# Optimization experiments

Measured on AMD Instinct MI355X. Metric: run time of the kernel, lower is better.

The kernel has to match this reference:

```python
import jax, jax.numpy as jnp
import numpy as np

N_NODES = 100000
N_EDGES = 1600000
IN_CH = 128
HID = 128
OUT_CH = 64
N_GRAPHS = 256


def setup_inputs() -> dict:
    key = jax.random.key(0)
    ks = jax.random.split(key, 12)
    x = jax.random.normal(ks[0], (N_NODES, IN_CH), dtype=jnp.float32)
    edge_index = jax.random.randint(ks[1], (2, N_EDGES), 0, N_NODES, dtype=jnp.int64)
    batch = jnp.sort(jax.random.randint(ks[2], (N_NODES,), 0, N_GRAPHS, dtype=jnp.int64))
    def glorot(k, shape):
        lim = np.sqrt(6.0 / (shape[0] + shape[1]))
        return jax.random.uniform(k, shape, jnp.float32, -lim, lim)
    w1 = glorot(ks[3], (IN_CH, HID)); b1 = jnp.zeros((HID,), jnp.float32)
    w2 = glorot(ks[4], (HID, HID));   b2 = jnp.zeros((HID,), jnp.float32)
    w3 = glorot(ks[5], (HID, HID));   b3 = jnp.zeros((HID,), jnp.float32)
    w_out = glorot(ks[6], (HID, OUT_CH)); b_out = jnp.zeros((OUT_CH,), jnp.float32)
    return {"x": x, "edge_index": edge_index, "batch": batch,
            "w1": w1, "b1": b1, "w2": w2, "b2": b2, "w3": w3, "b3": b3,
            "w_out": w_out, "b_out": b_out}


def reference(x, edge_index, batch, w1, b1, w2, b2, w3, b3, w_out, b_out):
    N = x.shape[0]
    # GCN normalization with added self-loops (PyG gcn_norm, symmetric):
    loop = jnp.arange(N, dtype=edge_index.dtype)
    src = jnp.concatenate([edge_index[0], loop])  # message source
    dst = jnp.concatenate([edge_index[1], loop])  # aggregate at target
    deg = jax.ops.segment_sum(jnp.ones(src.shape, jnp.float32), dst, num_segments=N)
    dinv = jax.lax.rsqrt(jnp.maximum(deg, 1.0))  # deg >= 1 due to self-loops
    norm = dinv[src] * dinv[dst]  # [E+N]

    def gcn_conv(h, w, b):
        h = h @ w  # transform first (PyG order)
        agg = jax.ops.segment_sum(norm[:, None] * h[src], dst, num_segments=N)
        return agg + b

    # norm module is None, dropout p=0 -> act-only branch, dropout no-op
    h = jax.nn.relu(gcn_conv(x, w1, b1))
    h = jax.nn.relu(gcn_conv(h, w2, b2))
    h = jax.nn.relu(gcn_conv(h, w3, b3))

    # global mean pool over graphs
    cnt = jax.ops.segment_sum(jnp.ones((N,), jnp.float32), batch, num_segments=N_GRAPHS)
    pooled = jax.ops.segment_sum(h, batch, num_segments=N_GRAPHS) / jnp.maximum(cnt, 1.0)[:, None]
    return pooled @ w_out + b_out  # [N_GRAPHS, OUT_CH]
```

## Files before the change

### kernel.cpp

```cpp
#include <hip/hip_runtime.h>
#include <hip/hip_fp16.h>

#define N_NODES 100000
#define N_EDGES 1600000
#define HID 128
#define OUT_CH 64
#define N_GRAPHS 256
#define CHUNK 1024
#define NCHUNK ((N_NODES + CHUNK - 1) / CHUNK)
#define NSLICE 8
#define SLICE_NODES ((N_NODES + NSLICE - 1) / NSLICE)

typedef _Float16 half8 __attribute__((ext_vector_type(8)));
typedef float f32x4 __attribute__((ext_vector_type(4)));

__global__ void k_init(int* cnt, float* pooled, float* gcnt) {
  int i = blockIdx.x * blockDim.x + threadIdx.x;
  int stride = gridDim.x * blockDim.x;
  for (int t = i; t < N_NODES; t += stride) cnt[t] = 0;
  for (int t = i; t < N_GRAPHS * HID; t += stride) pooled[t] = 0.f;
  for (int t = i; t < N_GRAPHS; t += stride) gcnt[t] = 0.f;
}

__global__ __launch_bounds__(256) void k_edge_count(const int* __restrict__ ei,
                                                    int* __restrict__ cnt) {
  int slice = blockIdx.x & (NSLICE - 1);
  int lo = slice * SLICE_NODES;
  int hi = min(lo + SLICE_NODES, N_NODES);
  int bi = blockIdx.x >> 3;
  int step = (gridDim.x >> 3) * 256;
  for (int e = bi * 256 + threadIdx.x; e < N_EDGES; e += step) {
    int d = ei[N_EDGES + e];
    if (d >= lo && d < hi) atomicAdd(&cnt[d], 1);
  }
}

__global__ void k_scan1(const int* __restrict__ cnt, int* __restrict__ row_ptr,
                        int* __restrict__ chunk_sums) {
  __shared__ int s[CHUNK];
  int t = threadIdx.x;
  int gid = blockIdx.x * CHUNK + t;
  int v = (gid < N_NODES) ? cnt[gid] : 0;
  s[t] = v;
  __syncthreads();
  for (int off = 1; off < CHUNK; off <<= 1) {
    int add = (t >= off) ? s[t - off] : 0;
    __syncthreads();
    s[t] += add;
    __syncthreads();
  }
  if (gid < N_NODES) row_ptr[gid] = s[t] - v;
  if (t == CHUNK - 1) chunk_sums[blockIdx.x] = s[t];
}

__global__ void k_scan2(const int* __restrict__ chunk_sums, int* __restrict__ chunk_off) {
  __shared__ int s[128];
  int t = threadIdx.x;
  int v = (t < NCHUNK) ? chunk_sums[t] : 0;
  s[t] = v;
  __syncthreads();
  for (int off = 1; off < 128; off <<= 1) {
    int add = (t >= off) ? s[t - off] : 0;
    __syncthreads();
    s[t] += add;
    __syncthreads();
  }
  if (t < NCHUNK) chunk_off[t] = s[t] - v;
}

__global__ void k_scan3(int* __restrict__ row_ptr, const int* __restrict__ chunk_off,
                        int* __restrict__ cursor, const int* __restrict__ cnt,
                        float* __restrict__ dinv) {
  int i = blockIdx.x * blockDim.x + threadIdx.x;
  if (i < N_NODES) {
    int v = row_ptr[i] + chunk_off[i / CHUNK];
    row_ptr[i] = v;
    cursor[i] = v;
    dinv[i] = rsqrtf((float)cnt[i] + 1.0f);
  }
  if (i == 0) row_ptr[N_NODES] = N_EDGES;
}

__global__ __launch_bounds__(256) void k_csr_fill(const int* __restrict__ ei,
                                                  const float* __restrict__ dinv,
                                                  int* __restrict__ cursor,
                                                  int2* __restrict__ E) {
  int slice = blockIdx.x & (NSLICE - 1);
  int lo = slice * SLICE_NODES;
  int hi = min(lo + SLICE_NODES, N_NODES);
  int bi = blockIdx.x >> 3;
  int step = (gridDim.x >> 3) * 256;
  for (int e = bi * 256 + threadIdx.x; e < N_EDGES; e += step) {
    int d = ei[N_EDGES + e];
    if (d >= lo && d < hi) {
      int s = ei[e];
      int p = atomicAdd(&cursor[d], 1);
      E[p] = make_int2(s, __float_as_int(dinv[s] * dinv[d]));
    }
  }
}

__global__ __launch_bounds__(256) void k_wtrans(const float* __restrict__ w1,
                                                const float* __restrict__ w2,
                                                const float* __restrict__ w3,
                                                __half* __restrict__ wt1,
                                                __half* __restrict__ wt2,
                                                __half* __restrict__ wt3) {
  int idx = blockIdx.x * 256 + threadIdx.x;
  int n = idx >> 7, k = idx & 127;
  const float* w = (blockIdx.y == 0) ? w1 : (blockIdx.y == 1) ? w2 : w3;
  __half* wt = (blockIdx.y == 0) ? wt1 : (blockIdx.y == 1) ? wt2 : wt3;
  wt[idx] = __float2half(w[k * HID + n]);
}

#define GBM 64
template <bool FP16IN>
__global__ __launch_bounds__(256) void k_gemm(const void* __restrict__ Hv,
                                              const __half* __restrict__ WT,
                                              __half* __restrict__ T) {
  __shared__ __half hs[GBM * HID];
  __shared__ __half ws[HID * HID];
  int tid = threadIdx.x;
  int m0 = blockIdx.x * GBM;

  for (int g = tid; g < GBM * 16; g += 256) {
    int r = g >> 4, kg = g & 15;
    int row = m0 + r;
    half8 h = {};
    if (row < N_NODES) {
      if constexpr (FP16IN) {
        h = *(const half8*)&((const _Float16*)Hv)[(size_t)row * HID + kg * 8];
      } else {
        const float* H = (const float*)Hv;
        float4 f0 = *(const float4*)&H[(size_t)row * HID + kg * 8];
        float4 f1 = *(const float4*)&H[(size_t)row * HID + kg * 8 + 4];
        h[0] = (_Float16)f0.x; h[1] = (_Float16)f0.y; h[2] = (_Float16)f0.z; h[3] = (_Float16)f0.w;
        h[4] = (_Float16)f1.x; h[5] = (_Float16)f1.y; h[6] = (_Float16)f1.z; h[7] = (_Float16)f1.w;
      }
    }
    int byte = (r * HID + kg * 8) * 2;
    byte ^= (r & 7) << 4;
    *(half8*)((char*)hs + byte) = h;
  }
  for (int g = tid; g < HID * 16; g += 256) {
    int n = g >> 4, kg = g & 15;
    half8 h = *(const half8*)&WT[n * HID + kg * 8];
    int byte = (n * HID + kg * 8) * 2;
    byte ^= (n & 7) << 4;
    *(half8*)((char*)ws + byte) = h;
  }
  __syncthreads();

  int w = tid >> 6, l = tid & 63;
  int r = (w << 4) + (l & 15);
  int kq = (l >> 4) << 3;
  f32x4 acc[8] = {};

  #pragma unroll
  for (int kc = 0; kc < HID; kc += 32) {
    int abyte = ((r * HID + kc + kq) * 2) ^ ((r & 7) << 4);
    half8 a = *(const half8*)((char*)hs + abyte);
    #pragma unroll
    for (int nb = 0; nb < 8; ++nb) {
      int n = nb * 16 + (l & 15);
      int bbyte = ((n * HID + kc + kq) * 2) ^ ((n & 7) << 4);
      half8 bfr = *(const half8*)((char*)ws + bbyte);
      acc[nb] = __builtin_amdgcn_mfma_f32_16x16x32_f16(a, bfr, acc[nb], 0, 0, 0);
    }
  }

  __syncthreads();
  #pragma unroll
  for (int nb = 0; nb < 8; ++nb) {
    #pragma unroll
    for (int j = 0; j < 4; ++j) {
      int rr = (w << 4) + ((l >> 4) << 2) + j;
      int cc = nb * 16 + (l & 15);
      int byte = (rr * HID + cc) * 2;
      byte ^= (rr & 7) << 4;
      *(__half*)((char*)hs + byte) = __float2half(acc[nb][j]);
    }
  }
  __syncthreads();
  for (int g = tid; g < GBM * 16; g += 256) {
    int rr = g >> 4, kg = g & 15;
    int byte = (rr * HID + kg * 8) * 2;
    byte ^= (rr & 7) << 4;
    half8 v = *(half8*)((char*)hs + byte);
    int row = m0 + rr;
    if (row < N_NODES)
      *(half8*)&((_Float16*)T)[(size_t)row * HID + kg * 8] = v;
  }
}

__device__ __forceinline__ void acc8(float* acc, uint4 v, float wt) {
  __half2 h0 = *(__half2*)&v.x, h1 = *(__half2*)&v.y;
  __half2 h2 = *(__half2*)&v.z, h3 = *(__half2*)&v.w;
  float2 f0 = __half22float2(h0), f1 = __half22float2(h1);
  float2 f2 = __half22float2(h2), f3 = __half22float2(h3);
  acc[0] += wt * f0.x; acc[1] += wt * f0.y;
  acc[2] += wt * f1.x; acc[3] += wt * f1.y;
  acc[4] += wt * f2.x; acc[5] += wt * f2.y;
  acc[6] += wt * f3.x; acc[7] += wt * f3.y;
}

__global__ __launch_bounds__(256) void k_agg(const __half* __restrict__ T,
                                             const int* __restrict__ row_ptr,
                                             const int2* __restrict__ E,
                                             const float* __restrict__ dinv,
                                             const float* __restrict__ bias,
                                             __half* __restrict__ Hout) {
  int wid = (blockIdx.x * blockDim.x + threadIdx.x) >> 6;
  int lane = threadIdx.x & 63;
  if (wid >= N_NODES) return;
  int q = lane >> 4;
  int wch = lane & 15;

  float acc[8] = {};
  float dn = dinv[wid];
  {
    uint4 vs = *(const uint4*)(T + (size_t)wid * HID + wch * 8);
    acc8(acc, vs, (q == 0) ? dn * dn : 0.f);
  }
  int p0 = row_ptr[wid], p1 = row_ptr[wid + 1];
  for (int p = p0; p < p1; p += 8) {
    int iA = p + q, iB = p + 4 + q;
    int cA = min(iA, p1 - 1), cB = min(iB, p1 - 1);
    int2 eA = E[cA];
    int2 eB = E[cB];
    uint4 vA = *(const uint4*)(T + (size_t)eA.x * HID + wch * 8);
    uint4 vB = *(const uint4*)(T + (size_t)eB.x * HID + wch * 8);
    float wA = (iA < p1) ? __int_as_float(eA.y) : 0.f;
    float wB = (iB < p1) ? __int_as_float(eB.y) : 0.f;
    acc8(acc, vA, wA);
    acc8(acc, vB, wB);
  }
  #pragma unroll
  for (int j = 0; j < 8; ++j) {
    acc[j] += __shfl_xor(acc[j], 16, 64);
    acc[j] += __shfl_xor(acc[j], 32, 64);
  }
  if (q == 0) {
    float4 b0 = *(const float4*)(bias + wch * 8);
    float4 b1 = *(const float4*)(bias + wch * 8 + 4);
    __half2 o0 = __floats2half2_rn(fmaxf(acc[0] + b0.x, 0.f), fmaxf(acc[1] + b0.y, 0.f));
    __half2 o1 = __floats2half2_rn(fmaxf(acc[2] + b0.z, 0.f), fmaxf(acc[3] + b0.w, 0.f));
    __half2 o2 = __floats2half2_rn(fmaxf(acc[4] + b1.x, 0.f), fmaxf(acc[5] + b1.y, 0.f));
    __half2 o3 = __floats2half2_rn(fmaxf(acc[6] + b1.z, 0.f), fmaxf(acc[7] + b1.w, 0.f));
    uint4 o;
    o.x = *(unsigned int*)&o0; o.y = *(unsigned int*)&o1;
    o.z = *(unsigned int*)&o2; o.w = *(unsigned int*)&o3;
    *(uint4*)(Hout + (size_t)wid * HID + wch * 8) = o;
  }
}

#define NODES_PER_BLOCK 64
__global__ __launch_bounds__(128) void k_pool(const __half* __restrict__ H,
                                              const int* __restrict__ batch,
                                              float* __restrict__ pooled,
                                              float* __restrict__ gcnt) {
  int c = threadIdx.x;
  int n0 = blockIdx.x * NODES_PER_BLOCK;
  if (n0 >= N_NODES) return;
  int n1 = min(n0 + NODES_PER_BLOCK, N_NODES);
  float sum = 0.f;
  float cntr = 0.f;
  int cur = batch[n0];
  for (int n = n0; n < n1; ++n) {
    int g = batch[n];
    if (g != cur) {
      atomicAdd(&pooled[cur * HID + c], sum);
      if (c == 0) atomicAdd(&gcnt[cur], cntr);
      sum = 0.f; cntr = 0.f; cur = g;
    }
    sum += __half2float(H[(size_t)n * HID + c]);
    cntr += 1.f;
  }
  atomicAdd(&pooled[cur * HID + c], sum);
  if (c == 0) atomicAdd(&gcnt[cur], cntr);
}

__global__ __launch_bounds__(64) void k_out(const float* __restrict__ pooled,
                                            const float* __restrict__ gcnt,
                                            const float* __restrict__ w_out,
                                            const float* __restrict__ b_out,
                                            float* __restrict__ out) {
  int g = blockIdx.x;
  int c = threadIdx.x;
  __shared__ float p[HID];
  float inv = 1.0f / fmaxf(gcnt[g], 1.0f);
  for (int k = c; k < HID; k += 64) p[k] = pooled[g * HID + k] * inv;
  __syncthreads();
  float acc = b_out[c];
  #pragma unroll 8
  for (int k = 0; k < HID; ++k) acc += p[k] * w_out[k * OUT_CH + c];
  out[g * OUT_CH + c] = acc;
}

extern "C" void kernel_launch(void* const* d_in, const int* in_sizes, int n_in,
                              void* d_out, int out_size, void* d_ws, size_t ws_size,
                              hipStream_t stream) {
  const float* x     = (const float*)d_in[0];
  const int*   ei    = (const int*)d_in[1];
  const int*   batch = (const int*)d_in[2];
  const float* w1    = (const float*)d_in[3];
  const float* b1    = (const float*)d_in[4];
  const float* w2    = (const float*)d_in[5];
  const float* b2    = (const float*)d_in[6];
  const float* w3    = (const float*)d_in[7];
  const float* b3    = (const float*)d_in[8];
  const float* w_out = (const float*)d_in[9];
  const float* b_out = (const float*)d_in[10];
  float* out = (float*)d_out;

  char* w = (char*)d_ws;
  auto alloc = [&](size_t bytes) { void* p = (void*)w; w += (bytes + 255) & ~(size_t)255; return p; };
  int*   cnt        = (int*)  alloc((size_t)N_NODES * 4);
  int*   row_ptr    = (int*)  alloc((size_t)(N_NODES + 1) * 4);
  int*   cursor     = (int*)  alloc((size_t)N_NODES * 4);
  float* dinv       = (float*)alloc((size_t)N_NODES * 4);
  int*   chunk_sums = (int*)  alloc((size_t)NCHUNK * 4);
  int*   chunk_off  = (int*)  alloc((size_t)NCHUNK * 4);
  int2*  E          = (int2*) alloc((size_t)N_EDGES * 8);
  __half* wt1       = (__half*)alloc((size_t)HID * HID * 2);
  __half* wt2       = (__half*)alloc((size_t)HID * HID * 2);
  __half* wt3       = (__half*)alloc((size_t)HID * HID * 2);
  __half* T         = (__half*)alloc((size_t)N_NODES * HID * 2);
  __half* Hh        = (__half*)alloc((size_t)N_NODES * HID * 2);
  float* pooled     = (float*)alloc((size_t)N_GRAPHS * HID * 4);
  float* gcnt       = (float*)alloc((size_t)N_GRAPHS * 4);

  const int NB = (N_NODES + 255) / 256;
  const int GB = (N_NODES + GBM - 1) / GBM;
  const int AB = (N_NODES + 3) / 4;
  const int PB = (N_NODES + NODES_PER_BLOCK - 1) / NODES_PER_BLOCK;

  k_init<<<256, 256, 0, stream>>>(cnt, pooled, gcnt);
  k_edge_count<<<2048, 256, 0, stream>>>(ei, cnt);
  k_scan1<<<NCHUNK, CHUNK, 0, stream>>>(cnt, row_ptr, chunk_sums);
  k_scan2<<<1, 128, 0, stream>>>(chunk_sums, chunk_off);
  k_scan3<<<NB, 256, 0, stream>>>(row_ptr, chunk_off, cursor, cnt, dinv);
  k_csr_fill<<<2048, 256, 0, stream>>>(ei, dinv, cursor, E);
  dim3 wtg(64, 3);
  k_wtrans<<<wtg, 256, 0, stream>>>(w1, w2, w3, wt1, wt2, wt3);

  k_gemm<false><<<GB, 256, 0, stream>>>(x, wt1, T);
  k_agg<<<AB, 256, 0, stream>>>(T, row_ptr, E, dinv, b1, Hh);
  k_gemm<true><<<GB, 256, 0, stream>>>(Hh, wt2, T);
  k_agg<<<AB, 256, 0, stream>>>(T, row_ptr, E, dinv, b2, Hh);
  k_gemm<true><<<GB, 256, 0, stream>>>(Hh, wt3, T);
  k_agg<<<AB, 256, 0, stream>>>(T, row_ptr, E, dinv, b3, Hh);

  k_pool<<<PB, 128, 0, stream>>>(Hh, batch, pooled, gcnt);
  k_out<<<N_GRAPHS, 64, 0, stream>>>(pooled, gcnt, w_out, b_out, out);
}
```

Baseline: 433.9 us.

## Bucket edges by destination slice before CSR build; store only sources

Adds a partition pass that stages each block's edges in shared memory and scatters them into per-slice buckets. The count and fill passes then read only their own bucket instead of each scanning all edges eight times. CSR entries shrink from (src, weight) pairs to bare source indices, and the aggregation kernel recomputes the edge weight from dinv[src] times the destination's dinv. This cuts edge-list traffic, at the cost of an extra kernel, extra bucket buffers with a fixed per-slice capacity, and an additional dinv gather per edge in aggregation.

```diff
diff --git a/kernel.cpp b/kernel.cpp
--- a/kernel.cpp
+++ b/kernel.cpp
@@ -10,29 +10,59 @@
 #define NCHUNK ((N_NODES + CHUNK - 1) / CHUNK)
 #define NSLICE 8
 #define SLICE_NODES ((N_NODES + NSLICE - 1) / NSLICE)
+#define CAPB 262144
+#define EPW 6250
 
 typedef _Float16 half8 __attribute__((ext_vector_type(8)));
 typedef float f32x4 __attribute__((ext_vector_type(4)));
 
-__global__ void k_init(int* cnt, float* pooled, float* gcnt) {
+__global__ void k_init(int* cnt, int* bcur, float* pooled, float* gcnt) {
   int i = blockIdx.x * blockDim.x + threadIdx.x;
   int stride = gridDim.x * blockDim.x;
   for (int t = i; t < N_NODES; t += stride) cnt[t] = 0;
+  for (int t = i; t < NSLICE; t += stride) bcur[t] = t * CAPB;
   for (int t = i; t < N_GRAPHS * HID; t += stride) pooled[t] = 0.f;
   for (int t = i; t < N_GRAPHS; t += stride) gcnt[t] = 0.f;
 }
 
-__global__ __launch_bounds__(256) void k_edge_count(const int* __restrict__ ei,
-                                                    int* __restrict__ cnt) {
-  int slice = blockIdx.x & (NSLICE - 1);
-  int lo = slice * SLICE_NODES;
-  int hi = min(lo + SLICE_NODES, N_NODES);
+__global__ __launch_bounds__(256) void k_part(const int* __restrict__ ei,
+                                              int* __restrict__ bcur,
+                                              int* __restrict__ bsrc,
+                                              int* __restrict__ bdst) {
+  __shared__ int2 stage[EPW];
+  __shared__ int hist[NSLICE], rbase[NSLICE], lcur[NSLICE];
+  int tid = threadIdx.x;
+  int e0 = blockIdx.x * EPW;
+  int n = min(EPW, N_EDGES - e0);
+  if (tid < NSLICE) { hist[tid] = 0; lcur[tid] = 0; }
+  __syncthreads();
+  for (int i = tid; i < n; i += 256) {
+    int s = ei[e0 + i], d = ei[N_EDGES + e0 + i];
+    stage[i] = make_int2(s, d);
+    atomicAdd(&hist[d / SLICE_NODES], 1);
+  }
+  __syncthreads();
+  if (tid < NSLICE) rbase[tid] = atomicAdd(&bcur[tid], hist[tid]);
+  __syncthreads();
+  for (int i = tid; i < n; i += 256) {
+    int2 e = stage[i];
+    int b = e.y / SLICE_NODES;
+    int p = rbase[b] + atomicAdd(&lcur[b], 1);
+    bsrc[p] = e.x;
+    bdst[p] = e.y;
+  }
+}
+
+__global__ __launch_bounds__(256) void k_count2(const int* __restrict__ bdst,
+                                                const int* __restrict__ bcur,
+                                                int* __restrict__ cnt) {
+  int b = blockIdx.x & (NSLICE - 1);
+  int base = b * CAPB;
+  int sz = bcur[b] - base;
   int bi = blockIdx.x >> 3;
   int step = (gridDim.x >> 3) * 256;
-  for (int e = bi * 256 + threadIdx.x; e < N_EDGES; e += step) {
-    int d = ei[N_EDGES + e];
-    if (d >= lo && d < hi) atomicAdd(&cnt[d], 1);
-  }
+  for (int i = bi * 256 + threadIdx.x; i < sz; i += step)
+    atomicAdd(&cnt[bdst[base + i]], 1);
 }
 
 __global__ void k_scan1(const int* __restrict__ cnt, int* __restrict__ row_ptr,
@@ -81,22 +111,20 @@
   if (i == 0) row_ptr[N_NODES] = N_EDGES;
 }
 
-__global__ __launch_bounds__(256) void k_csr_fill(const int* __restrict__ ei,
-                                                  const float* __restrict__ dinv,
-                                                  int* __restrict__ cursor,
-                                                  int2* __restrict__ E) {
-  int slice = blockIdx.x & (NSLICE - 1);
-  int lo = slice * SLICE_NODES;
-  int hi = min(lo + SLICE_NODES, N_NODES);
+__global__ __launch_bounds__(256) void k_fill2(const int* __restrict__ bsrc,
+                                               const int* __restrict__ bdst,
+                                               const int* __restrict__ bcur,
+                                               int* __restrict__ cursor,
+                                               int* __restrict__ E4) {
+  int b = blockIdx.x & (NSLICE - 1);
+  int base = b * CAPB;
+  int sz = bcur[b] - base;
   int bi = blockIdx.x >> 3;
   int step = (gridDim.x >> 3) * 256;
-  for (int e = bi * 256 + threadIdx.x; e < N_EDGES; e += step) {
-    int d = ei[N_EDGES + e];
-    if (d >= lo && d < hi) {
-      int s = ei[e];
-      int p = atomicAdd(&cursor[d], 1);
-      E[p] = make_int2(s, __float_as_int(dinv[s] * dinv[d]));
-    }
+  for (int i = bi * 256 + threadIdx.x; i < sz; i += step) {
+    int d = bdst[base + i];
+    int p = atomicAdd(&cursor[d], 1);
+    E4[p] = bsrc[base + i];
   }
 }
 
@@ -206,7 +234,7 @@
 
 __global__ __launch_bounds__(256) void k_agg(const __half* __restrict__ T,
                                              const int* __restrict__ row_ptr,
-                                             const int2* __restrict__ E,
+                                             const int* __restrict__ E4,
                                              const float* __restrict__ dinv,
                                              const float* __restrict__ bias,
                                              __half* __restrict__ Hout) {
@@ -226,12 +254,12 @@
   for (int p = p0; p < p1; p += 8) {
     int iA = p + q, iB = p + 4 + q;
     int cA = min(iA, p1 - 1), cB = min(iB, p1 - 1);
-    int2 eA = E[cA];
-    int2 eB = E[cB];
-    uint4 vA = *(const uint4*)(T + (size_t)eA.x * HID + wch * 8);
-    uint4 vB = *(const uint4*)(T + (size_t)eB.x * HID + wch * 8);
-    float wA = (iA < p1) ? __int_as_float(eA.y) : 0.f;
-    float wB = (iB < p1) ? __int_as_float(eB.y) : 0.f;
+    int sA = E4[cA];
+    int sB = E4[cB];
+    uint4 vA = *(const uint4*)(T + (size_t)sA * HID + wch * 8);
+    uint4 vB = *(const uint4*)(T + (size_t)sB * HID + wch * 8);
+    float wA = (iA < p1) ? dinv[sA] * dn : 0.f;
+    float wB = (iB < p1) ? dinv[sB] * dn : 0.f;
     acc8(acc, vA, wA);
     acc8(acc, vB, wB);
   }
@@ -321,7 +349,10 @@
   float* dinv       = (float*)alloc((size_t)N_NODES * 4);
   int*   chunk_sums = (int*)  alloc((size_t)NCHUNK * 4);
   int*   chunk_off  = (int*)  alloc((size_t)NCHUNK * 4);
-  int2*  E          = (int2*) alloc((size_t)N_EDGES * 8);
+  int*   bcur       = (int*)  alloc((size_t)NSLICE * 4);
+  int*   bsrc       = (int*)  alloc((size_t)NSLICE * CAPB * 4);
+  int*   bdst       = (int*)  alloc((size_t)NSLICE * CAPB * 4);
+  int*   E4         = (int*)  alloc((size_t)N_EDGES * 4);
   __half* wt1       = (__half*)alloc((size_t)HID * HID * 2);
   __half* wt2       = (__half*)alloc((size_t)HID * HID * 2);
   __half* wt3       = (__half*)alloc((size_t)HID * HID * 2);
@@ -334,22 +365,24 @@
   const int GB = (N_NODES + GBM - 1) / GBM;
   const int AB = (N_NODES + 3) / 4;
   const int PB = (N_NODES + NODES_PER_BLOCK - 1) / NODES_PER_BLOCK;
-
-  k_init<<<256, 256, 0, stream>>>(cnt, pooled, gcnt);
-  k_edge_count<<<2048, 256, 0, stream>>>(ei, cnt);
+  const int PARTB = (N_EDGES + EPW - 1) / EPW;
+
+  k_init<<<256, 256, 0, stream>>>(cnt, bcur, pooled, gcnt);
+  k_part<<<PARTB, 256, 0, stream>>>(ei, bcur, bsrc, bdst);
+  k_count2<<<2048, 256, 0, stream>>>(bdst, bcur, cnt);
   k_scan1<<<NCHUNK, CHUNK, 0, stream>>>(cnt, row_ptr, chunk_sums);
   k_scan2<<<1, 128, 0, stream>>>(chunk_sums, chunk_off);
   k_scan3<<<NB, 256, 0, stream>>>(row_ptr, chunk_off, cursor, cnt, dinv);
-  k_csr_fill<<<2048, 256, 0, stream>>>(ei, dinv, cursor, E);
+  k_fill2<<<2048, 256, 0, stream>>>(bsrc, bdst, bcur, cursor, E4);
   dim3 wtg(64, 3);
   k_wtrans<<<wtg, 256, 0, stream>>>(w1, w2, w3, wt1, wt2, wt3);
 
   k_gemm<false><<<GB, 256, 0, stream>>>(x, wt1, T);
-  k_agg<<<AB, 256, 0, stream>>>(T, row_ptr, E, dinv, b1, Hh);
+  k_agg<<<AB, 256, 0, stream>>>(T, row_ptr, E4, dinv, b1, Hh);
   k_gemm<true><<<GB, 256, 0, stream>>>(Hh, wt2, T);
-  k_agg<<<AB, 256, 0, stream>>>(T, row_ptr, E, dinv, b2, Hh);
+  k_agg<<<AB, 256, 0, stream>>>(T, row_ptr, E4, dinv, b2, Hh);
   k_gemm<true><<<GB, 256, 0, stream>>>(Hh, wt3, T);
-  k_agg<<<AB, 256, 0, stream>>>(T, row_ptr, E, dinv, b3, Hh);
+  k_agg<<<AB, 256, 0, stream>>>(T, row_ptr, E4, dinv, b3, Hh);
 
   k_pool<<<PB, 128, 0, stream>>>(Hh, batch, pooled, gcnt);
   k_out<<<N_GRAPHS, 64, 0, stream>>>(pooled, gcnt, w_out, b_out, out);
```

Result: slower. 450.2 us (+3.8%).
